# Optimization experiments

Measured on AMD Instinct MI355X. Metric: run time of the kernel, lower is better.

The kernel has to match this reference:

```python
import jax, jax.numpy as jnp
import numpy as np

N = 20000      # nodes
E = 256000     # edges
H = 8          # heads
DIN = 256      # in_dim_struct / in_dim_semantic
DH = 32        # num_hidden per head (H*DH == DIN for GT residual)
PRED = 32      # pred_dim (relation embedding dim)
REL = 16       # rel_num
NEG = 0.2      # negative_slope for GAT attention
ALPHA = 0.5    # args.fusion
NUM_LAYERS = 2


def seg_softmax(e, seg, n):
    # softmax over edges grouped by destination node; e: [E, ...], seg: [E]
    m = jax.ops.segment_max(e, seg, num_segments=n)
    ex = jnp.exp(e - m[seg])
    s = jax.ops.segment_sum(ex, seg, num_segments=n)
    return ex / (s[seg] + 1e-9)


def setup_inputs() -> dict:
    key = jax.random.key(0)
    ks = jax.random.split(key, 24)
    f32 = jnp.float32
    def rn(k, shape, scale=0.05):
        return jax.random.normal(k, shape, dtype=f32) * scale
    return {
        "feats_struct": jax.random.normal(ks[0], (N, DIN), f32),
        "feats_semantic": jax.random.normal(ks[1], (N, DIN), f32),
        "centrality": jax.random.uniform(ks[2], (N,), f32),
        # fused per-head scoring MLP (heads[0] small Sequentials batched over H)
        "Ws1": rn(ks[3], (H, DIN, DIN // 2)),
        "bs1": jnp.zeros((H, DIN // 2), f32),
        "Ws2": rn(ks[4], (H, DIN // 2)),
        "bs2": jnp.zeros((H,), f32),
        "rel_emb": rn(ks[5], (REL, PRED), 1.0),
        # SALayer params (2 layers, per-head scalar channels)
        "sa_w": rn(ks[6], (NUM_LAYERS, H), 1.0),
        "sa_al": rn(ks[7], (NUM_LAYERS, H), 1.0),
        "sa_ar": rn(ks[8], (NUM_LAYERS, H), 1.0),
        "sa_We": rn(ks[9], (NUM_LAYERS, PRED, H)),
        # GTLayer params
        "Wq": rn(ks[10], (DIN, H * DH)),
        "bq": jnp.zeros((H * DH,), f32),
        "Wk": rn(ks[11], (DIN, H * DH)),
        "bk": jnp.zeros((H * DH,), f32),
        "Wv": rn(ks[12], (DIN, H * DH)),
        "bv": jnp.zeros((H * DH,), f32),
        "We_gt": rn(ks[13], (PRED, H * DH)),
        "bn_gamma": jnp.ones((H * DH,), f32),
        "bn_beta": jnp.zeros((H * DH,), f32),
        "Wout": rn(ks[14], (H * DH, 1)),
        "bout": jnp.zeros((1,), f32),
        # centrality scale params
        "gamma": jnp.ones((1, H), f32),
        "beta": jnp.zeros((1, H), f32),
        "edge_types": jax.random.randint(ks[15], (E,), 0, REL),
        "edge_src": jax.random.randint(ks[16], (E,), 0, N),
        "edge_dst": jax.random.randint(ks[17], (E,), 0, N),
    }


def _forward(feats_struct, feats_semantic, centrality, Ws1, bs1, Ws2, bs2,
             rel_emb, sa_w, sa_al, sa_ar, sa_We, Wq, bq, Wk, bk, Wv, bv,
             We_gt, bn_gamma, bn_beta, Wout, bout, gamma, beta,
             edge_types, edge_src, edge_dst):
    n = feats_struct.shape[0]
    edge_feats = rel_emb[edge_types]                                   # [E, PRED]

    # ---- structural channel: fused per-head scoring MLPs ----
    h1 = jax.nn.relu(jnp.einsum('nd,hdk->nhk', feats_struct, Ws1) + bs1)  # [N,H,DIN/2]
    h = jnp.einsum('nhk,hk->nh', h1, Ws2) + bs2                           # [N,H]

    # ---- SALayer stack (GAT-style, per-head scalar features) ----
    for l in range(NUM_LAYERS):
        z = h * sa_w[l]                                                 # [N,H]
        e = jax.nn.leaky_relu(z[edge_src] * sa_al[l] + z[edge_dst] * sa_ar[l]
                              + edge_feats @ sa_We[l], NEG)             # [E,H]
        attn = seg_softmax(e, edge_dst, n)                              # [E,H]
        out = jax.ops.segment_sum(attn * z[edge_src], edge_dst, num_segments=n)
        h = jax.nn.elu(out + z)                                         # residual + activation
        if l != NUM_LAYERS - 1:
            h = jnp.mean(h, axis=-1, keepdims=True)
            h = jnp.tile(h, (1, H))
    logits_struct = h                                                   # [N,H]

    # ---- semantic channel: Graph Transformer layer (edge_mode='MUL') ----
    q = (feats_semantic @ Wq + bq).reshape(n, H, DH)
    k = (feats_semantic @ Wk + bk).reshape(n, H, DH)
    v = (feats_semantic @ Wv + bv).reshape(n, H, DH)
    ep = (edge_feats @ We_gt).reshape(-1, H, DH)                        # [E,H,DH]
    ke = k[edge_src] * ep                                               # MUL edge gating
    score = jnp.sum(q[edge_dst] * ke, axis=-1) / jnp.sqrt(jnp.float32(DH))  # [E,H]
    attn = seg_softmax(score, edge_dst, n)                              # [E,H]
    agg = jax.ops.segment_sum(attn[..., None] * v[edge_src], edge_dst,
                              num_segments=n).reshape(n, H * DH)
    agg = agg + feats_semantic                                          # residual (H*DH == DIN)
    mu = jnp.mean(agg, axis=0)
    var = jnp.var(agg, axis=0)
    agg = (agg - mu) / jnp.sqrt(var + 1e-5) * bn_gamma + bn_beta        # batch norm
    h_sem = jax.nn.relu(agg)
    logits_semantic = h_sem @ Wout + bout                               # [N,1]

    # ---- fusion + centrality gamma/beta scaling ----
    logits = ALPHA * logits_struct + (1.0 - ALPHA) * logits_semantic    # [N,H]
    scaled = (centrality[:, None] * gamma + beta) * logits              # [N,H]
    return jax.nn.leaky_relu(jnp.mean(scaled, axis=-1, keepdims=True), 0.01)


def reference(feats_struct, feats_semantic, centrality, Ws1, bs1, Ws2, bs2,
              rel_emb, sa_w, sa_al, sa_ar, sa_We, Wq, bq, Wk, bk, Wv, bv,
              We_gt, bn_gamma, bn_beta, Wout, bout, gamma, beta,
              edge_types, edge_src, edge_dst):
    return _forward(feats_struct, feats_semantic, centrality, Ws1, bs1, Ws2, bs2,
                    rel_emb, sa_w, sa_al, sa_ar, sa_We, Wq, bq, Wk, bk, Wv, bv,
                    We_gt, bn_gamma, bn_beta, Wout, bout, gamma, beta,
                    edge_types, edge_src, edge_dst)
```

## Files before the change

### kernel.cpp

```cpp
#include <hip/hip_runtime.h>
#include <hip/hip_bf16.h>
#include <math.h>

#define N_NODES 20000
#define N_EDGES 256000
#define LOG2E 1.4426950408889634f

typedef __attribute__((ext_vector_type(8))) __bf16 bf16x8;
typedef __attribute__((ext_vector_type(8))) unsigned short u16x8;
typedef __attribute__((ext_vector_type(4))) float f32x4;

static __device__ __forceinline__ unsigned short f2bf(float f) {
  unsigned u = __float_as_uint(f);
  unsigned r = (u + 0x7fffu + ((u >> 16) & 1u)) >> 16;
  return (unsigned short)r;
}
static __device__ __forceinline__ float b2f(unsigned short u) {
  return __uint_as_float((unsigned)u << 16);
}

__global__ __launch_bounds__(256) void k_setup(
    const float* __restrict__ rel_emb, const float* __restrict__ sa_We,
    const float* __restrict__ We_gt, const float* __restrict__ Xs,
    const float* __restrict__ Xm, const float* __restrict__ Ws1,
    const float* __restrict__ Wq, const float* __restrict__ Wk,
    const float* __restrict__ Wv, const int* __restrict__ e_dst,
    float* __restrict__ saTab, float* __restrict__ epTab,
    ushort* __restrict__ Xsb, ushort* __restrict__ Xmb,
    ushort* __restrict__ Ws1t, ushort* __restrict__ Wt,
    int* __restrict__ deg) {
  __shared__ float tl[32][33];
  int b = blockIdx.x;
  int t = threadIdx.x;
  if (b == 0) {
    {
      int l = t >> 7, r = (t >> 3) & 15, h = t & 7;
      float acc = 0.f;
      for (int p = 0; p < 32; ++p)
        acc += rel_emb[r * 32 + p] * sa_We[l * 256 + p * 8 + h];
      saTab[t] = acc * LOG2E;
    }
    for (int r = 0; r < 16; ++r) {
      float acc = 0.f;
      for (int p = 0; p < 32; ++p)
        acc += rel_emb[r * 32 + p] * We_gt[p * 256 + t];
      epTab[r * 256 + t] = acc;
    }
  } else if (b < 449) {
    int lb = b - 1;
    int r = t >> 5, c = t & 31;
    if (lb < 256) {
      int h = lb >> 5, idx = lb & 31;
      int k0 = (idx >> 3) * 32, d0 = (idx & 7) * 32;
      const float* src = Ws1 + (size_t)h * 32768;
      #pragma unroll
      for (int i = 0; i < 4; ++i)
        tl[r + i * 8][c] = src[(size_t)(d0 + r + i * 8) * 128 + k0 + c];
      __syncthreads();
      ushort* dst = Ws1t + (size_t)h * 32768;
      #pragma unroll
      for (int i = 0; i < 4; ++i)
        dst[(size_t)(k0 + r + i * 8) * 256 + d0 + c] = f2bf(tl[c][r + i * 8]);
    } else {
      int qi = lb - 256;
      int m = qi >> 6, idx = qi & 63;
      int n0 = (idx >> 3) * 32, d0 = (idx & 7) * 32;
      const float* src = (m == 0) ? Wq : (m == 1) ? Wk : Wv;
      #pragma unroll
      for (int i = 0; i < 4; ++i)
        tl[r + i * 8][c] = src[(size_t)(d0 + r + i * 8) * 256 + n0 + c];
      __syncthreads();
      ushort* dst = Wt + (size_t)m * 65536;
      #pragma unroll
      for (int i = 0; i < 4; ++i)
        dst[(size_t)(n0 + r + i * 8) * 256 + d0 + c] = f2bf(tl[c][r + i * 8]);
    }
  } else if (b < 5449) {
    size_t i = ((size_t)(b - 449) * 256 + t) * 4;
    float4 a = *(const float4*)(Xs + i);
    ushort4 ua = {f2bf(a.x), f2bf(a.y), f2bf(a.z), f2bf(a.w)};
    *(ushort4*)(Xsb + i) = ua;
    float4 c4 = *(const float4*)(Xm + i);
    ushort4 uc = {f2bf(c4.x), f2bf(c4.y), f2bf(c4.z), f2bf(c4.w)};
    *(ushort4*)(Xmb + i) = uc;
  } else {
    int e = (b - 5449) * 256 + t;
    if (e < N_EDGES) atomicAdd(&deg[e_dst[e]], 1);
  }
}

__global__ __launch_bounds__(1024) void k_scan(const int* __restrict__ deg,
                                               int* __restrict__ rowPtr,
                                               int* __restrict__ cursor) {
  const int CH = (N_NODES + 1023) / 1024;
  int t = threadIdx.x;
  int b0 = t * CH, b1 = min(b0 + CH, N_NODES);
  int s = 0;
  for (int i = b0; i < b1; ++i) s += deg[i];
  __shared__ int part[1024];
  part[t] = s;
  __syncthreads();
  for (int off = 1; off < 1024; off <<= 1) {
    int add = (t >= off) ? part[t - off] : 0;
    __syncthreads();
    part[t] += add;
    __syncthreads();
  }
  int run = (t == 0) ? 0 : part[t - 1];
  for (int i = b0; i < b1; ++i) {
    rowPtr[i] = run;
    cursor[i] = run;
    run += deg[i];
  }
  if (t == 0) rowPtr[N_NODES] = part[1023];
}

__global__ void k_fill(const int* __restrict__ e_dst, const int* __restrict__ e_src,
                       const int* __restrict__ e_type, int* __restrict__ cursor,
                       int2* __restrict__ csrPack) {
  int e = blockIdx.x * 256 + threadIdx.x;
  if (e >= N_EDGES) return;
  int d = e_dst[e];
  int pos = atomicAdd(&cursor[d], 1);
  csrPack[pos] = make_int2(e_src[e], e_type[e]);
}

__global__ __launch_bounds__(512) void k_gemm(
    const ushort* __restrict__ Xsb, const ushort* __restrict__ Xmb,
    const ushort* __restrict__ Ws1t, const ushort* __restrict__ Wqkvt,
    const float* __restrict__ bs1, const float* __restrict__ Ws2,
    const float* __restrict__ bs2, const float* __restrict__ bq,
    const float* __restrict__ bk, const float* __restrict__ bv,
    float* __restrict__ h0, float* __restrict__ q, ushort* __restrict__ kvB) {
  __shared__ ushort Ab[128][256];
  __shared__ ushort Bb[128][256];
  int tid = threadIdx.x;
  int y = blockIdx.y;
  bool isMlp = (y < 8);
  int m = 0, half = 0;
  const ushort* Bsrc;
  const ushort* Xb;
  if (isMlp) {
    Xb = Xsb;
    Bsrc = Ws1t + (size_t)y * 128 * 256;
  } else {
    int s = y - 8;
    m = s >> 1;
    half = s & 1;
    Xb = Xmb;
    Bsrc = Wqkvt + ((size_t)m * 256 + half * 128) * 256;
  }
  int base = blockIdx.x * 128;

  {
    int r = tid >> 2, cq = (tid & 3) * 8;
    int gr = base + r;
    const ushort* asrc = Xb + (size_t)gr * 256;
    const ushort* bsrc = Bsrc + (size_t)r * 256;
    int sw = (r & 7) << 3;
    #pragma unroll
    for (int s = 0; s < 8; ++s) {
      int colc = (cq + s) * 8;
      int csw = colc ^ sw;
      u16x8 av = {0, 0, 0, 0, 0, 0, 0, 0};
      if (gr < N_NODES) av = *(const u16x8*)(asrc + colc);
      *(u16x8*)&Ab[r][csw] = av;
      *(u16x8*)&Bb[r][csw] = *(const u16x8*)(bsrc + colc);
    }
  }
  __syncthreads();

  int wv = tid >> 6, lane = tid & 63;
  int l15 = lane & 15, lhi = lane >> 4;
  int swzA = (l15 & 7) << 3;
  f32x4 acc[8];
  #pragma unroll
  for (int nt = 0; nt < 8; ++nt) acc[nt] = (f32x4){0.f, 0.f, 0.f, 0.f};

  #pragma unroll
  for (int kk = 0; kk < 8; ++kk) {
    int col = kk * 32 + lhi * 8;
    bf16x8 a = *(const bf16x8*)&Ab[wv * 16 + l15][col ^ swzA];
    #pragma unroll
    for (int nt = 0; nt < 8; ++nt) {
      bf16x8 b = *(const bf16x8*)&Bb[nt * 16 + l15][col ^ swzA];
      acc[nt] = __builtin_amdgcn_mfma_f32_16x16x32_bf16(a, b, acc[nt], 0, 0, 0);
    }
  }

  if (isMlp) {
    float part[4] = {0.f, 0.f, 0.f, 0.f};
    #pragma unroll
    for (int nt = 0; nt < 8; ++nt) {
      int c = y * 128 + nt * 16 + l15;
      float b1 = bs1[c], w2 = Ws2[c];
      #pragma unroll
      for (int j = 0; j < 4; ++j)
        part[j] += fmaxf(acc[nt][j] + b1, 0.f) * w2;
    }
    #pragma unroll
    for (int j = 0; j < 4; ++j) {
      #pragma unroll
      for (int o = 1; o < 16; o <<= 1) part[j] += __shfl_xor(part[j], o);
    }
    if (l15 == 0) {
      float b2 = bs2[y];
      #pragma unroll
      for (int j = 0; j < 4; ++j) {
        int row = base + wv * 16 + lhi * 4 + j;
        if (row < N_NODES) h0[(size_t)row * 8 + y] = part[j] + b2;
      }
    }
  } else {
    const float* bias = (m == 0) ? bq : (m == 1) ? bk : bv;
    #pragma unroll
    for (int nt = 0; nt < 8; ++nt) {
      int c = half * 128 + nt * 16 + l15;
      float bc = bias[c];
      #pragma unroll
      for (int j = 0; j < 4; ++j) {
        int row = base + wv * 16 + lhi * 4 + j;
        if (row < N_NODES) {
          float val = acc[nt][j] + bc;
          if (m == 0) q[(size_t)row * 256 + c] = val;
          else if (m == 1) kvB[(size_t)row * 512 + c] = f2bf(val);
          else kvB[(size_t)row * 512 + 256 + c] = f2bf(val);
        }
      }
    }
  }
}


__global__ __launch_bounds__(256) void k_sa(const float* __restrict__ h_in,
                                            float* __restrict__ h_out,
                                            const int* __restrict__ rowPtr,
                                            const int2* __restrict__ csrPack,
                                            const float* __restrict__ sa_w,
                                            const float* __restrict__ sa_al,
                                            const float* __restrict__ sa_ar,
                                            const float* __restrict__ saTab, int layer) {
  int node = blockIdx.x * 4 + (threadIdx.x >> 6);
  int lane = threadIdx.x & 63;
  int h = lane & 7, eslot = lane >> 3;
  float wgt = sa_w[layer * 8 + h];
  float al2 = sa_al[layer * 8 + h] * LOG2E;
  float ar2 = sa_ar[layer * 8 + h] * LOG2E;
  const float* tab = saTab + layer * 128;
  float zd = h_in[(size_t)node * 8 + h] * wgt;
  int s0 = rowPtr[node], s1 = rowPtr[node + 1];
  float m = -1e30f, lsum = 0.f, acc = 0.f;
  for (int i = s0 + eslot; i < s1; i += 8) {
    int2 p = csrPack[i];
    float zs = h_in[(size_t)p.x * 8 + h] * wgt;
    float e = zs * al2 + zd * ar2 + tab[p.y * 8 + h];
    e = (e >= 0.f) ? e : 0.2f * e;
    float nm = fmaxf(m, e);
    float scl = exp2f(m - nm);
    float pw = exp2f(e - nm);
    acc = acc * scl + pw * zs;
    lsum = lsum * scl + pw;
    m = nm;
  }
  #pragma unroll
  for (int off = 8; off < 64; off <<= 1) {
    float om = __shfl_xor(m, off);
    float ol = __shfl_xor(lsum, off);
    float oa = __shfl_xor(acc, off);
    float nm = fmaxf(m, om);
    float sl = exp2f(m - nm);
    float so = exp2f(om - nm);
    acc = acc * sl + oa * so;
    lsum = lsum * sl + ol * so;
    m = nm;
  }
  float o = acc / (lsum + 1e-9f);
  float r = o + zd;
  r = (r > 0.f) ? r : expm1f(r);
  if (layer == 0) {
    r += __shfl_xor(r, 1);
    r += __shfl_xor(r, 2);
    r += __shfl_xor(r, 4);
    r *= 0.125f;
  }
  if (eslot == 0) h_out[(size_t)node * 8 + h] = r;
}


__global__ __launch_bounds__(256) void k_gt(const float* __restrict__ q,
                                            const ushort* __restrict__ kvB,
                                            const float* __restrict__ epTab,
                                            const float* __restrict__ feats_sem,
                                            const int* __restrict__ rowPtr,
                                            const int2* __restrict__ csrPack,
                                            ushort* __restrict__ agg) {
  int node = blockIdx.x * 4 + (threadIdx.x >> 6);
  int lane = threadIdx.x & 63;
  int c0 = lane * 4;
  const float SC2 = 0.17677669529663687f * LOG2E;
  float4 qv = *(const float4*)(q + (size_t)node * 256 + c0);
  qv.x *= SC2; qv.y *= SC2; qv.z *= SC2; qv.w *= SC2;
  float4 acc = {0.f, 0.f, 0.f, 0.f};
  float m = -1e30f, lsum = 0.f;
  int s0 = rowPtr[node], s1 = rowPtr[node + 1];
  int i = s0;
  for (; i + 1 < s1; i += 2) {
    int2 eA = csrPack[i], eB = csrPack[i + 1];
    const ushort* rA = kvB + (size_t)eA.x * 512 + c0;
    const ushort* rB = kvB + (size_t)eB.x * 512 + c0;
    ushort4 kA = *(const ushort4*)rA;
    ushort4 kB4 = *(const ushort4*)rB;
    float4 epA = *(const float4*)(epTab + eA.y * 256 + c0);
    float4 epB = *(const float4*)(epTab + eB.y * 256 + c0);
    ushort4 vA = *(const ushort4*)(rA + 256);
    ushort4 vB = *(const ushort4*)(rB + 256);
    float pA = qv.x * b2f(kA.x) * epA.x + qv.y * b2f(kA.y) * epA.y +
               qv.z * b2f(kA.z) * epA.z + qv.w * b2f(kA.w) * epA.w;
    float pB = qv.x * b2f(kB4.x) * epB.x + qv.y * b2f(kB4.y) * epB.y +
               qv.z * b2f(kB4.z) * epB.z + qv.w * b2f(kB4.w) * epB.w;
    pA += __shfl_xor(pA, 1); pB += __shfl_xor(pB, 1);
    pA += __shfl_xor(pA, 2); pB += __shfl_xor(pB, 2);
    pA += __shfl_xor(pA, 4); pB += __shfl_xor(pB, 4);
    float nm = fmaxf(m, fmaxf(pA, pB));
    float scl = exp2f(m - nm);
    float wA = exp2f(pA - nm);
    float wB = exp2f(pB - nm);
    acc.x = acc.x * scl + wA * b2f(vA.x) + wB * b2f(vB.x);
    acc.y = acc.y * scl + wA * b2f(vA.y) + wB * b2f(vB.y);
    acc.z = acc.z * scl + wA * b2f(vA.z) + wB * b2f(vB.z);
    acc.w = acc.w * scl + wA * b2f(vA.w) + wB * b2f(vB.w);
    lsum = lsum * scl + wA + wB;
    m = nm;
  }
  if (i < s1) {
    int2 eA = csrPack[i];
    const ushort* rA = kvB + (size_t)eA.x * 512 + c0;
    ushort4 kv = *(const ushort4*)rA;
    float4 ep = *(const float4*)(epTab + eA.y * 256 + c0);
    ushort4 vv = *(const ushort4*)(rA + 256);
    float part = qv.x * b2f(kv.x) * ep.x + qv.y * b2f(kv.y) * ep.y +
                 qv.z * b2f(kv.z) * ep.z + qv.w * b2f(kv.w) * ep.w;
    part += __shfl_xor(part, 1);
    part += __shfl_xor(part, 2);
    part += __shfl_xor(part, 4);
    float nm = fmaxf(m, part);
    float scl = exp2f(m - nm);
    float pw = exp2f(part - nm);
    acc.x = acc.x * scl + pw * b2f(vv.x);
    acc.y = acc.y * scl + pw * b2f(vv.y);
    acc.z = acc.z * scl + pw * b2f(vv.z);
    acc.w = acc.w * scl + pw * b2f(vv.w);
    lsum = lsum * scl + pw;
    m = nm;
  }
  float inv = 1.f / (lsum + 1e-9f);
  float4 fs = *(const float4*)(feats_sem + (size_t)node * 256 + c0);
  ushort4 r;
  r.x = f2bf(acc.x * inv + fs.x);
  r.y = f2bf(acc.y * inv + fs.y);
  r.z = f2bf(acc.z * inv + fs.z);
  r.w = f2bf(acc.w * inv + fs.w);
  *(ushort4*)(agg + (size_t)node * 256 + c0) = r;
}

__global__ void k_bnstats(const ushort* __restrict__ agg, double* __restrict__ colsum,
                          double* __restrict__ colssq) {
  int t = threadIdx.x;
  int r0 = blockIdx.x * 79;
  int r1 = min(r0 + 79, N_NODES);
  double s = 0.0, qq = 0.0;
  for (int r = r0; r < r1; ++r) {
    float x = b2f(agg[(size_t)r * 256 + t]);
    s += (double)x;
    qq += (double)x * (double)x;
  }
  atomicAdd(&colsum[t], s);
  atomicAdd(&colssq[t], qq);
}

__global__ void k_bnfinal(const double* __restrict__ colsum, const double* __restrict__ colssq,
                          float* __restrict__ muArr, float* __restrict__ invArr) {
  int t = threadIdx.x;
  double mu = colsum[t] / (double)N_NODES;
  double var = colssq[t] / (double)N_NODES - mu * mu;
  muArr[t] = (float)mu;
  invArr[t] = (float)(1.0 / sqrt(var + 1e-5));
}

__global__ __launch_bounds__(256) void k_final(const ushort* __restrict__ agg,
                                               const float* __restrict__ muArr,
                                               const float* __restrict__ invArr,
                                               const float* __restrict__ bn_gamma,
                                               const float* __restrict__ bn_beta,
                                               const float* __restrict__ Wout,
                                               const float* __restrict__ bout,
                                               const float* __restrict__ hB,
                                               const float* __restrict__ cent,
                                               const float* __restrict__ gamma,
                                               const float* __restrict__ beta,
                                               float* __restrict__ out) {
  int node = blockIdx.x * 4 + (threadIdx.x >> 6);
  int lane = threadIdx.x & 63;
  int c0 = lane * 4;
  ushort4 xa = *(const ushort4*)(agg + (size_t)node * 256 + c0);
  float4 mu = *(const float4*)(muArr + c0);
  float4 iv = *(const float4*)(invArr + c0);
  float4 g = *(const float4*)(bn_gamma + c0);
  float4 b = *(const float4*)(bn_beta + c0);
  float4 w = *(const float4*)(Wout + c0);
  float p = fmaxf((b2f(xa.x) - mu.x) * iv.x * g.x + b.x, 0.f) * w.x +
            fmaxf((b2f(xa.y) - mu.y) * iv.y * g.y + b.y, 0.f) * w.y +
            fmaxf((b2f(xa.z) - mu.z) * iv.z * g.z + b.z, 0.f) * w.z +
            fmaxf((b2f(xa.w) - mu.w) * iv.w * g.w + b.w, 0.f) * w.w;
  #pragma unroll
  for (int o = 1; o < 64; o <<= 1) p += __shfl_xor(p, o);
  float ls = p + bout[0];
  int h = lane & 7;
  float logit = 0.5f * hB[(size_t)node * 8 + h] + 0.5f * ls;
  float sc = (cent[node] * gamma[h] + beta[h]) * logit;
  sc += __shfl_xor(sc, 1);
  sc += __shfl_xor(sc, 2);
  sc += __shfl_xor(sc, 4);
  float mn = sc * 0.125f;
  mn = (mn >= 0.f) ? mn : 0.01f * mn;
  if (lane == 0) out[node] = mn;
}


extern "C" void kernel_launch(void* const* d_in, const int* in_sizes, int n_in,
                              void* d_out, int out_size, void* d_ws, size_t ws_size,
                              hipStream_t stream) {
  (void)in_sizes; (void)n_in; (void)out_size; (void)ws_size;
  const float* feats_struct = (const float*)d_in[0];
  const float* feats_sem    = (const float*)d_in[1];
  const float* cent         = (const float*)d_in[2];
  const float* Ws1          = (const float*)d_in[3];
  const float* bs1          = (const float*)d_in[4];
  const float* Ws2          = (const float*)d_in[5];
  const float* bs2          = (const float*)d_in[6];
  const float* rel_emb      = (const float*)d_in[7];
  const float* sa_w         = (const float*)d_in[8];
  const float* sa_al        = (const float*)d_in[9];
  const float* sa_ar        = (const float*)d_in[10];
  const float* sa_We        = (const float*)d_in[11];
  const float* Wq           = (const float*)d_in[12];
  const float* bq           = (const float*)d_in[13];
  const float* Wk           = (const float*)d_in[14];
  const float* bk           = (const float*)d_in[15];
  const float* Wv           = (const float*)d_in[16];
  const float* bv           = (const float*)d_in[17];
  const float* We_gt        = (const float*)d_in[18];
  const float* bn_gamma     = (const float*)d_in[19];
  const float* bn_beta      = (const float*)d_in[20];
  const float* Wout         = (const float*)d_in[21];
  const float* bout         = (const float*)d_in[22];
  const float* gamma        = (const float*)d_in[23];
  const float* beta         = (const float*)d_in[24];
  const int* e_type         = (const int*)d_in[25];
  const int* e_src          = (const int*)d_in[26];
  const int* e_dst          = (const int*)d_in[27];
  float* out = (float*)d_out;

  char* wsb = (char*)d_ws;
  size_t off = 0;
  auto alloc = [&](size_t bytes) -> char* {
    char* p = wsb + off;
    off = (off + bytes + 255) & ~(size_t)255;
    return p;
  };
  float* saTab   = (float*)alloc(2 * 16 * 8 * 4);
  float* epTab   = (float*)alloc(16 * 256 * 4);
  int* deg       = (int*)alloc((size_t)N_NODES * 4);
  int* rowPtr    = (int*)alloc((size_t)(N_NODES + 1) * 4);
  int* cursor    = (int*)alloc((size_t)N_NODES * 4);
  int2* csrPack  = (int2*)alloc((size_t)N_EDGES * 8);
  float* h0      = (float*)alloc((size_t)N_NODES * 8 * 4);
  float* hA      = (float*)alloc((size_t)N_NODES * 8 * 4);
  float* hB      = (float*)alloc((size_t)N_NODES * 8 * 4);
  float* qb      = (float*)alloc((size_t)N_NODES * 256 * 4);
  ushort* kvB    = (ushort*)alloc((size_t)N_NODES * 512 * 2);
  ushort* agg    = (ushort*)alloc((size_t)N_NODES * 256 * 2);
  double* colsum = (double*)alloc(256 * 8);
  double* colssq = (double*)alloc(256 * 8);
  float* muArr   = (float*)alloc(256 * 4);
  float* invArr  = (float*)alloc(256 * 4);
  ushort* Xsb    = (ushort*)alloc((size_t)N_NODES * 256 * 2);
  ushort* Xmb    = (ushort*)alloc((size_t)N_NODES * 256 * 2);
  ushort* Ws1t   = (ushort*)alloc((size_t)8 * 128 * 256 * 2);
  ushort* Wqkvt  = (ushort*)alloc((size_t)3 * 256 * 256 * 2);

  hipMemsetAsync(deg, 0, (size_t)N_NODES * 4, stream);
  hipMemsetAsync(colsum, 0, 256 * 8, stream);
  hipMemsetAsync(colssq, 0, 256 * 8, stream);

  k_setup<<<6449, 256, 0, stream>>>(rel_emb, sa_We, We_gt, feats_struct, feats_sem,
                                    Ws1, Wq, Wk, Wv, e_dst,
                                    saTab, epTab, Xsb, Xmb, Ws1t, Wqkvt, deg);
  k_scan<<<1, 1024, 0, stream>>>(deg, rowPtr, cursor);
  k_fill<<<(N_EDGES + 255) / 256, 256, 0, stream>>>(e_dst, e_src, e_type, cursor, csrPack);

  const int MT = (N_NODES + 127) / 128;
  dim3 gGemm(MT, 14);
  k_gemm<<<gGemm, 512, 0, stream>>>(Xsb, Xmb, Ws1t, Wqkvt, bs1, Ws2, bs2,
                                    bq, bk, bv, h0, qb, kvB);
  k_sa<<<(N_NODES + 3) / 4, 256, 0, stream>>>(h0, hA, rowPtr, csrPack,
                                              sa_w, sa_al, sa_ar, saTab, 0);
  k_sa<<<(N_NODES + 3) / 4, 256, 0, stream>>>(hA, hB, rowPtr, csrPack,
                                              sa_w, sa_al, sa_ar, saTab, 1);
  k_gt<<<N_NODES / 4, 256, 0, stream>>>(qb, kvB, epTab, feats_sem,
                                        rowPtr, csrPack, agg);
  k_bnstats<<<256, 256, 0, stream>>>(agg, colsum, colssq);
  k_bnfinal<<<1, 256, 0, stream>>>(colsum, colssq, muArr, invArr);
  k_final<<<N_NODES / 4, 256, 0, stream>>>(agg, muArr, invArr, bn_gamma, bn_beta,
                                           Wout, bout, hB, cent, gamma, beta, out);
}
```

Before: 414.2 us.

## Keep A tile in registers and loop over weight slices in GEMM

Restructures the projection GEMM so each block loads its 64-row activation tile once into registers and loops over all weight slices (8 MLP heads or 6 QKV halves). Previously every block reloaded 128 rows of activations for each of 14 grid columns. The activation rereads from global memory go away, but each block now runs serially through the slices with syncs between B reloads and has no double buffering. The grid also shrinks to 2 columns, which lowers parallelism and makes the two columns uneven (8 slices versus 6).

```diff
diff --git a/kernel.cpp b/kernel.cpp
--- a/kernel.cpp
+++ b/kernel.cpp
@@ -125,106 +125,108 @@
   csrPack[pos] = make_int2(e_src[e], e_type[e]);
 }
 
-__global__ __launch_bounds__(512) void k_gemm(
+__global__ __launch_bounds__(256) void k_gemm(
     const ushort* __restrict__ Xsb, const ushort* __restrict__ Xmb,
     const ushort* __restrict__ Ws1t, const ushort* __restrict__ Wqkvt,
     const float* __restrict__ bs1, const float* __restrict__ Ws2,
     const float* __restrict__ bs2, const float* __restrict__ bq,
     const float* __restrict__ bk, const float* __restrict__ bv,
     float* __restrict__ h0, float* __restrict__ q, ushort* __restrict__ kvB) {
-  __shared__ ushort Ab[128][256];
   __shared__ ushort Bb[128][256];
   int tid = threadIdx.x;
   int y = blockIdx.y;
-  bool isMlp = (y < 8);
-  int m = 0, half = 0;
-  const ushort* Bsrc;
-  const ushort* Xb;
-  if (isMlp) {
-    Xb = Xsb;
-    Bsrc = Ws1t + (size_t)y * 128 * 256;
-  } else {
-    int s = y - 8;
-    m = s >> 1;
-    half = s & 1;
-    Xb = Xmb;
-    Bsrc = Wqkvt + ((size_t)m * 256 + half * 128) * 256;
-  }
-  int base = blockIdx.x * 128;
-
-  {
-    int r = tid >> 2, cq = (tid & 3) * 8;
-    int gr = base + r;
-    const ushort* asrc = Xb + (size_t)gr * 256;
-    const ushort* bsrc = Bsrc + (size_t)r * 256;
-    int sw = (r & 7) << 3;
-    #pragma unroll
-    for (int s = 0; s < 8; ++s) {
-      int colc = (cq + s) * 8;
-      int csw = colc ^ sw;
-      u16x8 av = {0, 0, 0, 0, 0, 0, 0, 0};
-      if (gr < N_NODES) av = *(const u16x8*)(asrc + colc);
-      *(u16x8*)&Ab[r][csw] = av;
-      *(u16x8*)&Bb[r][csw] = *(const u16x8*)(bsrc + colc);
-    }
-  }
-  __syncthreads();
-
+  int base = blockIdx.x * 64;
   int wv = tid >> 6, lane = tid & 63;
   int l15 = lane & 15, lhi = lane >> 4;
-  int swzA = (l15 & 7) << 3;
-  f32x4 acc[8];
-  #pragma unroll
-  for (int nt = 0; nt < 8; ++nt) acc[nt] = (f32x4){0.f, 0.f, 0.f, 0.f};
-
-  #pragma unroll
-  for (int kk = 0; kk < 8; ++kk) {
-    int col = kk * 32 + lhi * 8;
-    bf16x8 a = *(const bf16x8*)&Ab[wv * 16 + l15][col ^ swzA];
+  int rowbase = base + wv * 16;
+
+  const ushort* Xb = (y == 0) ? Xsb : Xmb;
+  bf16x8 A[8];
+  {
+    int row = rowbase + l15;
+    bool ok = row < N_NODES;
+    const ushort* rp = Xb + (size_t)row * 256;
     #pragma unroll
-    for (int nt = 0; nt < 8; ++nt) {
-      bf16x8 b = *(const bf16x8*)&Bb[nt * 16 + l15][col ^ swzA];
-      acc[nt] = __builtin_amdgcn_mfma_f32_16x16x32_bf16(a, b, acc[nt], 0, 0, 0);
-    }
-  }
-
-  if (isMlp) {
-    float part[4] = {0.f, 0.f, 0.f, 0.f};
+    for (int kk = 0; kk < 8; ++kk) {
+      u16x8 v = {0, 0, 0, 0, 0, 0, 0, 0};
+      if (ok) v = *(const u16x8*)(rp + kk * 32 + lhi * 8);
+      A[kk] = *(bf16x8*)&v;
+    }
+  }
+
+  int nSlices = (y == 0) ? 8 : 6;
+  int swz = (l15 & 7) << 3;
+  for (int sl = 0; sl < nSlices; ++sl) {
+    const ushort* Bsrc;
+    if (y == 0) {
+      Bsrc = Ws1t + (size_t)sl * 128 * 256;
+    } else {
+      int m = sl >> 1, half = sl & 1;
+      Bsrc = Wqkvt + ((size_t)m * 256 + half * 128) * 256;
+    }
+    __syncthreads();
     #pragma unroll
-    for (int nt = 0; nt < 8; ++nt) {
-      int c = y * 128 + nt * 16 + l15;
-      float b1 = bs1[c], w2 = Ws2[c];
-      #pragma unroll
-      for (int j = 0; j < 4; ++j)
-        part[j] += fmaxf(acc[nt][j] + b1, 0.f) * w2;
-    }
+    for (int ps = 0; ps < 16; ++ps) {
+      int r = ps * 8 + (tid >> 5);
+      int ce = (tid & 31) * 8;
+      int csw = ce ^ ((r & 7) << 3);
+      *(u16x8*)&Bb[r][csw] = *(const u16x8*)(Bsrc + (size_t)r * 256 + ce);
+    }
+    __syncthreads();
+
+    f32x4 acc[8];
     #pragma unroll
-    for (int j = 0; j < 4; ++j) {
-      #pragma unroll
-      for (int o = 1; o < 16; o <<= 1) part[j] += __shfl_xor(part[j], o);
-    }
-    if (l15 == 0) {
-      float b2 = bs2[y];
+    for (int nt = 0; nt < 8; ++nt) acc[nt] = (f32x4){0.f, 0.f, 0.f, 0.f};
+    #pragma unroll
+    for (int kk = 0; kk < 8; ++kk) {
+      int col = kk * 32 + lhi * 8;
+      #pragma unroll
+      for (int nt = 0; nt < 8; ++nt) {
+        bf16x8 b = *(const bf16x8*)&Bb[nt * 16 + l15][col ^ swz];
+        acc[nt] = __builtin_amdgcn_mfma_f32_16x16x32_bf16(A[kk], b, acc[nt], 0, 0, 0);
+      }
+    }
+
+    if (y == 0) {
+      int h = sl;
+      float part[4] = {0.f, 0.f, 0.f, 0.f};
+      #pragma unroll
+      for (int nt = 0; nt < 8; ++nt) {
+        int c = h * 128 + nt * 16 + l15;
+        float b1 = bs1[c], w2 = Ws2[c];
+        #pragma unroll
+        for (int j = 0; j < 4; ++j)
+          part[j] += fmaxf(acc[nt][j] + b1, 0.f) * w2;
+      }
       #pragma unroll
       for (int j = 0; j < 4; ++j) {
-        int row = base + wv * 16 + lhi * 4 + j;
-        if (row < N_NODES) h0[(size_t)row * 8 + y] = part[j] + b2;
+        #pragma unroll
+        for (int o = 1; o < 16; o <<= 1) part[j] += __shfl_xor(part[j], o);
       }
-    }
-  } else {
-    const float* bias = (m == 0) ? bq : (m == 1) ? bk : bv;
-    #pragma unroll
-    for (int nt = 0; nt < 8; ++nt) {
-      int c = half * 128 + nt * 16 + l15;
-      float bc = bias[c];
-      #pragma unroll
-      for (int j = 0; j < 4; ++j) {
-        int row = base + wv * 16 + lhi * 4 + j;
-        if (row < N_NODES) {
-          float val = acc[nt][j] + bc;
-          if (m == 0) q[(size_t)row * 256 + c] = val;
-          else if (m == 1) kvB[(size_t)row * 512 + c] = f2bf(val);
-          else kvB[(size_t)row * 512 + 256 + c] = f2bf(val);
+      if (l15 == 0) {
+        float b2 = bs2[h];
+        #pragma unroll
+        for (int j = 0; j < 4; ++j) {
+          int row = rowbase + lhi * 4 + j;
+          if (row < N_NODES) h0[(size_t)row * 8 + h] = part[j] + b2;
+        }
+      }
+    } else {
+      int m = sl >> 1, half = sl & 1;
+      const float* bias = (m == 0) ? bq : (m == 1) ? bk : bv;
+      #pragma unroll
+      for (int nt = 0; nt < 8; ++nt) {
+        int c = half * 128 + nt * 16 + l15;
+        float bc = bias[c];
+        #pragma unroll
+        for (int j = 0; j < 4; ++j) {
+          int row = rowbase + lhi * 4 + j;
+          if (row < N_NODES) {
+            float val = acc[nt][j] + bc;
+            if (m == 0) q[(size_t)row * 256 + c] = val;
+            else if (m == 1) kvB[(size_t)row * 512 + c] = f2bf(val);
+            else kvB[(size_t)row * 512 + 256 + c] = f2bf(val);
+          }
         }
       }
     }
@@ -499,9 +501,9 @@
   k_scan<<<1, 1024, 0, stream>>>(deg, rowPtr, cursor);
   k_fill<<<(N_EDGES + 255) / 256, 256, 0, stream>>>(e_dst, e_src, e_type, cursor, csrPack);
 
-  const int MT = (N_NODES + 127) / 128;
-  dim3 gGemm(MT, 14);
-  k_gemm<<<gGemm, 512, 0, stream>>>(Xsb, Xmb, Ws1t, Wqkvt, bs1, Ws2, bs2,
+  const int MT = (N_NODES + 63) / 64;
+  dim3 gGemm(MT, 2);
+  k_gemm<<<gGemm, 256, 0, stream>>>(Xsb, Xmb, Ws1t, Wqkvt, bs1, Ws2, bs2,
                                     bq, bk, bv, h0, qb, kvB);
   k_sa<<<(N_NODES + 3) / 4, 256, 0, stream>>>(h0, hA, rowPtr, csrPack,
                                               sa_w, sa_al, sa_ar, saTab, 0);
```

New measurement: 365.0 us. -11.9%, faster.
